# Kernel optimization log

Hardware: AMD Instinct MI355X
Metric: run time of the kernel (lower is better)

Reference implementation:

```python
import jax, jax.numpy as jnp
import numpy as np

NC = 1      # constants.nc (Game-of-Life grid channels)
GRID = 32
PAD_ITERS = 31


def _iterated_wrap_idx(n, p):
    # Faithfully simulate p iterations of circular pad-1 on a growing axis.
    # NOTE: this is NOT a single wrap-pad of p; the border alternates 0/n-1.
    idx = np.arange(n)
    for _ in range(p):
        idx = np.concatenate([idx[-1:], idx, idx[:1]])
    return jnp.asarray(idx)

_IDX = _iterated_wrap_idx(GRID, PAD_ITERS)  # length 94, static


def _pad(x):
    # one gather per spatial dim replaces the 31-iteration concat loop
    return x[:, :, _IDX][:, :, :, _IDX]


def _conv(x, w, b, stride):
    y = jax.lax.conv_general_dilated(
        x, w, window_strides=(stride, stride), padding='VALID',
        dimension_numbers=('NCHW', 'OIHW', 'NCHW'))
    return y + b[None, :, None, None]


def setup_inputs() -> dict:
    key = jax.random.key(0)
    ks = jax.random.split(key, 7)
    B = 16
    s_in = 1.0 / np.sqrt(NC * 32 * 32)      # fan-in init, keeps activations sane
    s_hid = 1.0 / np.sqrt(32 * 32 * 32)
    s_out = 1.0 / np.sqrt(32)
    return {
        'x': jax.random.normal(ks[0], (B, NC, GRID, GRID), jnp.float32),
        'in_w': jax.random.normal(ks[1], (32, NC, 32, 32), jnp.float32) * s_in,
        'in_b': jnp.zeros((32,), jnp.float32),
        'convs_w': jax.random.normal(ks[2], (20, 32, 32, 32, 32), jnp.float32) * s_hid,
        'convs_b': jnp.zeros((20, 32), jnp.float32),
        'out_w': jax.random.normal(ks[3], (NC, 32, 1, 1), jnp.float32) * s_out,
        'out_b': jnp.zeros((NC,), jnp.float32),
    }


def reference(x, in_w, in_b, convs_w, convs_b, out_w, out_b):
    # in_conv: pad(31 iters) + conv k=32 s=2 (no ReLU, as in original)
    h = _conv(_pad(x), in_w, in_b, 2)           # [B,32,32,32]

    def step(h, wb):
        w, b = wb
        h = jax.nn.relu(_conv(_pad(h), w, b, 2))
        return h, None

    h, _ = jax.lax.scan(step, h, (convs_w, convs_b))  # 20 hidden layers
    return _conv(h, out_w, out_b, 1)             # 1x1 out conv, no activation
```

## Files before the change

kernel.cpp:

```cpp
#include <hip/hip_runtime.h>


typedef _Float16 f16;
typedef _Float16 f16x8 __attribute__((ext_vector_type(8)));
typedef float f32x4 __attribute__((ext_vector_type(4)));
typedef float f32x16 __attribute__((ext_vector_type(16)));

__device__ __forceinline__ int mwrap(int j) {
  int t = j - 31;
  if ((unsigned)t <= 31u) return t;
  if (t < 0) return (j & 1) ? 0 : 31;
  return (j & 1) ? 0 : 31;
}


template <int CIN, bool RELU, bool PRE>
__global__ __launch_bounds__(512, 2) void gemm3(
    const void* __restrict__ Wv,
    const f16* __restrict__ hp_in,
    const float* __restrict__ bias,
    f16* __restrict__ hp_out) {
  __shared__ __align__(16) f16 rowbuf[2][32][96];
  __shared__ float Red[8][2][1024];

  const int tid = threadIdx.x;
  const int lane = tid & 63;
  const int w = tid >> 6;
  const int ox = lane & 31;
  const int s = lane >> 5;

  const int pair0 = blockIdx.x * 2;
  const int b = pair0 >> 5;
  const int oy0 = pair0 & 31;

  const int rrow = tid / 12, rseg = tid - rrow * 12;

  f32x16 acc0 = {}, acc1 = {};
  f16x8 Acur[8], Anxt[8];
  f16x8 stg = {};

  auto loadA = [&](int c, f16x8* dst) {
#pragma unroll
    for (int kyi = 0; kyi < 4; ++kyi) {
#pragma unroll
      for (int kxh = 0; kxh < 2; ++kxh) {
        const int ky = w + 8 * kyi;
        const int chunk = (c * 32 + ky) * 2 + kxh;
        if constexpr (PRE) {
          const f16* Wl = (const f16*)Wv;
          dst[kyi * 2 + kxh] = *(const f16x8*)(Wl + (size_t)chunk * 512 + lane * 8);
        } else {
          const float* Wl = (const float*)Wv;
          const float* sp = Wl + (((size_t)(ox * CIN + c) * 32 + ky) * 32 + kxh * 16 + s * 8);
          f32x4 u0 = *(const f32x4*)sp;
          f32x4 u1 = *(const f32x4*)(sp + 4);
          f16x8 v;
          v[0] = (f16)u0[0]; v[1] = (f16)u0[1]; v[2] = (f16)u0[2]; v[3] = (f16)u0[3];
          v[4] = (f16)u1[0]; v[5] = (f16)u1[1]; v[6] = (f16)u1[2]; v[7] = (f16)u1[3];
          dst[kyi * 2 + kxh] = v;
        }
      }
    }
  };
  auto loadRow = [&](int c) {
    if (tid < 384)
      stg = *(const f16x8*)(hp_in + ((size_t)(b * CIN + c) * 32 + rrow) * 96 + rseg * 8);
  };
  auto writeRow = [&](int nb) {
    if (tid < 384) *(f16x8*)(&rowbuf[nb][rrow][rseg * 8]) = stg;
  };

  loadA(0, Acur);
  loadRow(0);
  writeRow(0);
  __syncthreads();

  for (int c = 0; c < CIN; ++c) {
    const int buf = c & 1;
    if (c + 1 < CIN) {
      loadA(c + 1, Anxt);
      loadRow(c + 1);
    }
#pragma unroll
    for (int kyi = 0; kyi < 4; ++kyi) {
      const int ky = w + 8 * kyi;
      const int y0 = mwrap(2 * oy0 + ky);
      const int y1 = mwrap(2 * (oy0 + 1) + ky);
      const int* R0 = (const int*)(&rowbuf[buf][y0][0]);
      const int* R1 = (const int*)(&rowbuf[buf][y1][0]);
#pragma unroll
      for (int kxh = 0; kxh < 2; ++kxh) {
        const int bi = ox + 4 * s + 8 * kxh;
        int4 b0w, b1w;
        b0w.x = R0[bi]; b0w.y = R0[bi + 1]; b0w.z = R0[bi + 2]; b0w.w = R0[bi + 3];
        b1w.x = R1[bi]; b1w.y = R1[bi + 1]; b1w.z = R1[bi + 2]; b1w.w = R1[bi + 3];
        f16x8 bf0 = __builtin_bit_cast(f16x8, b0w);
        f16x8 bf1 = __builtin_bit_cast(f16x8, b1w);
        const f16x8 a = Acur[kyi * 2 + kxh];
        acc0 = __builtin_amdgcn_mfma_f32_32x32x16_f16(a, bf0, acc0, 0, 0, 0);
        acc1 = __builtin_amdgcn_mfma_f32_32x32x16_f16(a, bf1, acc1, 0, 0, 0);
      }
    }
    if (c + 1 < CIN) {
      writeRow(buf ^ 1);
#pragma unroll
      for (int u = 0; u < 8; ++u) Acur[u] = Anxt[u];
    }
    __syncthreads();
  }

#pragma unroll
  for (int r = 0; r < 16; ++r) {
    Red[w][0][r * 64 + lane] = acc0[r];
    Red[w][1][r * 64 + lane] = acc1[r];
  }
  __syncthreads();

#pragma unroll
  for (int k4 = 0; k4 < 4; ++k4) {
    const int o = tid + 512 * k4;
    const int p = o >> 10, co = (o >> 5) & 31, oxx = o & 31;
    const int idx = ((co & 3) + 4 * (co >> 3)) * 64 + ((co >> 2) & 1) * 32 + oxx;
    float v = bias[co];
#pragma unroll
    for (int w8 = 0; w8 < 8; ++w8) v += Red[w8][p][idx];
    if (RELU) v = fmaxf(v, 0.f);
    const f16 hv = (f16)v;
    f16* base = hp_out + ((size_t)(b * 32 + co) * 32 + (oy0 + p)) * 96;
    base[oxx + 31] = hv;
    if (oxx == 0) {
#pragma unroll
      for (int j = 1; j <= 29; j += 2) base[j] = hv;
#pragma unroll
      for (int j = 63; j <= 93; j += 2) base[j] = hv;
    }
    if (oxx == 31) {
#pragma unroll
      for (int j = 0; j <= 30; j += 2) base[j] = hv;
#pragma unroll
      for (int j = 64; j <= 92; j += 2) base[j] = hv;
    }
  }
}

__global__ void pad_x_kernel(const float* __restrict__ x, f16* __restrict__ xp) {
  const int i = blockIdx.x * 256 + threadIdx.x;
  if (i >= 48128) return;
  const int bq = i / 3008, r = i - bq * 3008;
  const int y = r / 94, j = r - y * 94;
  xp[bq * 3072 + y * 96 + j] = (f16)x[(bq * 32 + y) * 32 + mwrap(j)];
}

__global__ void convert_w3(const float* __restrict__ in_w,
                           const float* __restrict__ convs_w,
                           f16* __restrict__ WfIn, f16* __restrict__ WfH) {
  const int total = 4096 + 20 * 131072;
  for (int g = blockIdx.x * blockDim.x + threadIdx.x; g < total;
       g += gridDim.x * blockDim.x) {
    const float* src;
    f16* dst;
    int chunk, lanE, c, ky, kxh;
    if (g < 4096) {
      chunk = g >> 6; lanE = g & 63;
      kxh = chunk & 1; ky = chunk >> 1; c = 0;
      const int co = lanE & 31, ss = lanE >> 5;
      src = in_w + ((size_t)(co * 1 + 0) * 32 + ky) * 32 + kxh * 16 + ss * 8;
      dst = WfIn + (size_t)chunk * 512 + lanE * 8;
    } else {
      const int h = g - 4096;
      const int layer = h >> 17, r = h & 131071;
      chunk = r >> 6; lanE = r & 63;
      kxh = chunk & 1;
      const int t = chunk >> 1;
      ky = t & 31; c = t >> 5;
      const int co = lanE & 31, ss = lanE >> 5;
      src = convs_w + (size_t)layer * 1048576 +
            ((size_t)(co * 32 + c) * 32 + ky) * 32 + kxh * 16 + ss * 8;
      dst = WfH + (size_t)layer * 1048576 + (size_t)chunk * 512 + lanE * 8;
    }
    f32x4 u0 = *(const f32x4*)src;
    f32x4 u1 = *(const f32x4*)(src + 4);
    f16x8 v;
    v[0] = (f16)u0[0]; v[1] = (f16)u0[1]; v[2] = (f16)u0[2]; v[3] = (f16)u0[3];
    v[4] = (f16)u1[0]; v[5] = (f16)u1[1]; v[6] = (f16)u1[2]; v[7] = (f16)u1[3];
    *(f16x8*)dst = v;
  }
}

__global__ void out_conv3(const f16* __restrict__ hp,
                          const float* __restrict__ ow,
                          const float* __restrict__ ob,
                          float* __restrict__ out) {
  const int o = blockIdx.x * 256 + threadIdx.x;
  const int b = o >> 10, oy = (o >> 5) & 31, oxx = o & 31;
  float s = ob[0];
#pragma unroll
  for (int c = 0; c < 32; ++c)
    s += ow[c] * (float)hp[((size_t)(b * 32 + c) * 32 + oy) * 96 + oxx + 31];
  out[o] = s;
}

extern "C" void kernel_launch(void* const* d_in, const int* in_sizes, int n_in,
                              void* d_out, int out_size, void* d_ws,
                              size_t ws_size, hipStream_t stream) {
  const float* x = (const float*)d_in[0];
  const float* in_w = (const float*)d_in[1];
  const float* in_b = (const float*)d_in[2];
  const float* convs_w = (const float*)d_in[3];
  const float* convs_b = (const float*)d_in[4];
  const float* out_w = (const float*)d_in[5];
  const float* out_b = (const float*)d_in[6];
  float* out = (float*)d_out;

  char* ws = (char*)d_ws;
  f16* xpad = (f16*)ws;
  f16* hpA = (f16*)(ws + 98304);
  f16* hpB = (f16*)(ws + 98304 + 3145728);
  f16* WfIn = (f16*)(ws + 6389760);
  f16* WfH = (f16*)(ws + 6455296);
  const bool pre = (ws_size >= 48398336ull);

  pad_x_kernel<<<188, 256, 0, stream>>>(x, xpad);
  if (pre) convert_w3<<<2048, 256, 0, stream>>>(in_w, convs_w, WfIn, WfH);

  if (pre)
    gemm3<1, false, true><<<256, 512, 0, stream>>>(WfIn, xpad, in_b, hpA);
  else
    gemm3<1, false, false><<<256, 512, 0, stream>>>(in_w, xpad, in_b, hpA);

  for (int l = 0; l < 20; ++l) {
    const f16* cur = (l % 2 == 0) ? hpA : hpB;
    f16* nxt = (l % 2 == 0) ? hpB : hpA;
    if (pre)
      gemm3<32, true, true><<<256, 512, 0, stream>>>(
          WfH + (size_t)l * 1048576, cur, convs_b + 32 * l, nxt);
    else
      gemm3<32, true, false><<<256, 512, 0, stream>>>(
          convs_w + (size_t)l * 1048576, cur, convs_b + 32 * l, nxt);
  }

  out_conv3<<<64, 256, 0, stream>>>(hpA, out_w, out_b, out);
}
```

Measured before the change: 1.003 ms.

## Reassign ky per wave to share row fragments between output rows

Each wave now handles four consecutive ky values (4*w+kyi) instead of strided ones. Because the two output rows sit two input rows apart, their B fragments overlap and only six LDS row reads are needed instead of eight, with row indices precomputed outside the loop. The channel loop is unrolled by two with ping-pong A registers, which removes the Anxt to Acur copy. A raw s_barrier with explicit waitcnt and sched barriers replaces __syncthreads to control instruction ordering. This adds register pressure and relies on hand-placed scheduling hints.

```diff
diff --git a/kernel.cpp b/kernel.cpp
--- a/kernel.cpp
+++ b/kernel.cpp
@@ -35,8 +35,12 @@
 
   const int rrow = tid / 12, rseg = tid - rrow * 12;
 
+  int ybase[6];
+#pragma unroll
+  for (int j = 0; j < 6; ++j) ybase[j] = mwrap(2 * oy0 + 4 * w + j);
+
   f32x16 acc0 = {}, acc1 = {};
-  f16x8 Acur[8], Anxt[8];
+  f16x8 A0[8], A1[8];
   f16x8 stg = {};
 
   auto loadA = [&](int c, f16x8* dst) {
@@ -44,7 +48,7 @@
     for (int kyi = 0; kyi < 4; ++kyi) {
 #pragma unroll
       for (int kxh = 0; kxh < 2; ++kxh) {
-        const int ky = w + 8 * kyi;
+        const int ky = 4 * w + kyi;
         const int chunk = (c * 32 + ky) * 2 + kxh;
         if constexpr (PRE) {
           const f16* Wl = (const f16*)Wv;
@@ -70,43 +74,54 @@
     if (tid < 384) *(f16x8*)(&rowbuf[nb][rrow][rseg * 8]) = stg;
   };
 
-  loadA(0, Acur);
+  auto body = [&](int c, const f16x8* Ause, f16x8* Apre) {
+    const int buf = c & 1;
+    const bool pre = (c + 1 < CIN);
+    if (pre) {
+      loadRow(c + 1);
+      __builtin_amdgcn_sched_barrier(0);
+      loadA(c + 1, Apre);
+    }
+    f16x8 F[6][2];
+#pragma unroll
+    for (int j = 0; j < 6; ++j) {
+      const int* R = (const int*)(&rowbuf[buf][ybase[j]][0]);
+#pragma unroll
+      for (int kxh = 0; kxh < 2; ++kxh) {
+        const int bi = ox + 4 * s + 8 * kxh;
+        int4 t;
+        t.x = R[bi]; t.y = R[bi + 1]; t.z = R[bi + 2]; t.w = R[bi + 3];
+        F[j][kxh] = __builtin_bit_cast(f16x8, t);
+      }
+    }
+#pragma unroll
+    for (int kyi = 0; kyi < 4; ++kyi) {
+#pragma unroll
+      for (int kxh = 0; kxh < 2; ++kxh) {
+        const f16x8 a = Ause[kyi * 2 + kxh];
+        acc0 = __builtin_amdgcn_mfma_f32_32x32x16_f16(a, F[kyi][kxh], acc0, 0, 0, 0);
+        acc1 = __builtin_amdgcn_mfma_f32_32x32x16_f16(a, F[kyi + 2][kxh], acc1, 0, 0, 0);
+      }
+    }
+    if (pre) writeRow(buf ^ 1);
+    asm volatile("s_waitcnt lgkmcnt(0)" ::: "memory");
+    __builtin_amdgcn_sched_barrier(0);
+    __builtin_amdgcn_s_barrier();
+  };
+
+  loadA(0, A0);
   loadRow(0);
   writeRow(0);
   __syncthreads();
 
-  for (int c = 0; c < CIN; ++c) {
-    const int buf = c & 1;
-    if (c + 1 < CIN) {
-      loadA(c + 1, Anxt);
-      loadRow(c + 1);
-    }
-#pragma unroll
-    for (int kyi = 0; kyi < 4; ++kyi) {
-      const int ky = w + 8 * kyi;
-      const int y0 = mwrap(2 * oy0 + ky);
-      const int y1 = mwrap(2 * (oy0 + 1) + ky);
-      const int* R0 = (const int*)(&rowbuf[buf][y0][0]);
-      const int* R1 = (const int*)(&rowbuf[buf][y1][0]);
-#pragma unroll
-      for (int kxh = 0; kxh < 2; ++kxh) {
-        const int bi = ox + 4 * s + 8 * kxh;
-        int4 b0w, b1w;
-        b0w.x = R0[bi]; b0w.y = R0[bi + 1]; b0w.z = R0[bi + 2]; b0w.w = R0[bi + 3];
-        b1w.x = R1[bi]; b1w.y = R1[bi + 1]; b1w.z = R1[bi + 2]; b1w.w = R1[bi + 3];
-        f16x8 bf0 = __builtin_bit_cast(f16x8, b0w);
-        f16x8 bf1 = __builtin_bit_cast(f16x8, b1w);
-        const f16x8 a = Acur[kyi * 2 + kxh];
-        acc0 = __builtin_amdgcn_mfma_f32_32x32x16_f16(a, bf0, acc0, 0, 0, 0);
-        acc1 = __builtin_amdgcn_mfma_f32_32x32x16_f16(a, bf1, acc1, 0, 0, 0);
-      }
-    }
-    if (c + 1 < CIN) {
-      writeRow(buf ^ 1);
-#pragma unroll
-      for (int u = 0; u < 8; ++u) Acur[u] = Anxt[u];
-    }
-    __syncthreads();
+  if constexpr (CIN == 1) {
+    body(0, A0, A1);
+  } else {
+#pragma unroll 1
+    for (int c = 0; c < CIN; c += 2) {
+      body(c, A0, A1);
+      body(c + 1, A1, A0);
+    }
   }
 
 #pragma unroll
```

After: 978.6 us. -2.4%, faster.
